# Kernel optimization log

Hardware: AMD Instinct MI355X
Metric: run time of the kernel (lower is better)

Reference implementation:

```python
import jax, jax.numpy as jnp
import numpy as np

B, N, E = 2, 50000, 400000
FIN, HID, OUT = 128, 128, 128
EPS = 1e-5  # BatchNorm1d default eps


def setup_inputs() -> dict:
    key = jax.random.key(0)
    ks = jax.random.split(key, 12)
    x = jax.random.normal(ks[0], (B, N, FIN), dtype=jnp.float32)
    row = jax.random.randint(ks[1], (E,), 0, N, dtype=jnp.int32)          # scatter dst
    col = jnp.concatenate([jnp.arange(N, dtype=jnp.int32),                # ensure deg>=1
                           jax.random.randint(ks[2], (E - N,), 0, N, dtype=jnp.int32)])
    edge_index = jnp.stack([row, col])                                    # [2, E]
    deg = jnp.zeros((N,), jnp.float32).at[col].add(1.0)                   # degree(col, N)
    dis = deg ** -0.5
    norm = (dis[row] * dis[col])[None, :, None]                           # [1, E, 1]
    W1 = jax.random.normal(ks[3], (HID, FIN), jnp.float32) / np.sqrt(FIN)
    b1 = jax.random.normal(ks[4], (HID,), jnp.float32) * 0.01
    g1 = jnp.ones((N,), jnp.float32)
    be1 = jnp.zeros((N,), jnp.float32)
    W2 = jax.random.normal(ks[5], (OUT, HID), jnp.float32) / np.sqrt(HID)
    b2 = jax.random.normal(ks[6], (OUT,), jnp.float32) * 0.01
    g2 = jnp.ones((N,), jnp.float32)
    be2 = jnp.zeros((N,), jnp.float32)
    return {"x": x, "edge_index": edge_index, "norm": norm,
            "W1": W1, "b1": b1, "g1": g1, "be1": be1,
            "W2": W2, "b2": b2, "g2": g2, "be2": be2}


def _gcn_layer(x, edge_index, norm, W, b, g, be):
    # Linear (dropout p=0 -> identity)
    h = jnp.einsum('bnf,of->bno', x, W) + b                 # [B, N, C]
    # BatchNorm1d(num_features=N): per-node stats over (batch, channel)
    mu = jnp.mean(h, axis=(0, 2), keepdims=True)            # [1, N, 1]
    var = jnp.var(h, axis=(0, 2), keepdims=True)            # biased, as torch
    y = g[None, :, None] * (h - mu) * jax.lax.rsqrt(var + EPS) + be[None, :, None]
    a = jax.nn.gelu(y, approximate=False)                   # torch GELU = exact erf
    # message passing: gather src nodes, scale by norm, scatter-add to dst
    msgs = a[:, edge_index[1], :] * norm                    # [B, E, C]
    return jnp.zeros_like(a).at[:, edge_index[0], :].add(msgs)


def reference(x, edge_index, norm, W1, b1, g1, be1, W2, b2, g2, be2):
    x = _gcn_layer(x, edge_index, norm, W1, b1, g1, be1)
    x = _gcn_layer(x, edge_index, norm, W2, b2, g2, be2)
    return x
```

## Files before the change

kernel.cpp:

```cpp
#include <hip/hip_runtime.h>
#include <math.h>

#define CC 128

typedef unsigned short u16;
typedef short bf16x8 __attribute__((ext_vector_type(8)));
typedef float f32x4 __attribute__((ext_vector_type(4)));

typedef __attribute__((address_space(3))) void lds_t;
typedef const __attribute__((address_space(1))) void gbl_t;

__device__ __forceinline__ u16 f2bf(float f) {
    union { float f; unsigned u; } v; v.f = f;
    unsigned u = v.u;
    return (u16)((u + 0x7FFFu + ((u >> 16) & 1u)) >> 16);
}
__device__ __forceinline__ float bf2f(unsigned hi16) {
    union { unsigned u; float f; } v; v.u = hi16 << 16; return v.f;
}
__device__ __forceinline__ unsigned cvt_pk(float lo, float hi) {
    unsigned r;
    asm("v_cvt_pk_bf16_f32 %0, %1, %2" : "=v"(r) : "v"(lo), "v"(hi));
    return r;
}

__device__ __forceinline__ float gelu_f(float y) {
    float xa = fabsf(y) * 0.70710678118654752f;
    float t  = __builtin_amdgcn_rcpf(fmaf(0.3275911f, xa, 1.0f));
    float p  = fmaf(1.061405429f, t, -1.453152027f);
    p = fmaf(p, t, 1.421413741f);
    p = fmaf(p, t, -0.284496736f);
    p = fmaf(p, t, 0.254829592f);
    p *= t;
    float e  = __expf(-xa * xa);
    float er = fmaf(-p, e, 1.0f);
    float s  = copysignf(er, y);
    return 0.5f * y * (1.0f + s);
}


__global__ __launch_bounds__(256) void k_zero_i32(int* __restrict__ p, int n) {
    int i = blockIdx.x * 256 + threadIdx.x;
    if (i < n) p[i] = 0;
}

__global__ __launch_bounds__(256) void k_hist(const int* __restrict__ row, int* __restrict__ cnt, int E) {
    int e = blockIdx.x * 256 + threadIdx.x;
    if (e < E) atomicAdd(&cnt[row[e]], 1);
}

__device__ __forceinline__ int wave_incl_scan(int v) {
    #pragma unroll
    for (int d = 1; d < 64; d <<= 1) {
        int t = __shfl_up(v, d);
        if ((threadIdx.x & 63) >= d) v += t;
    }
    return v;
}

__global__ __launch_bounds__(256) void k_scan_a(const int* __restrict__ cnt, int* __restrict__ bsum, int N) {
    int base = blockIdx.x * 1024 + threadIdx.x * 4;
    int s = 0;
    #pragma unroll
    for (int u = 0; u < 4; ++u) { int i = base + u; if (i < N) s += cnt[i]; }
    #pragma unroll
    for (int d = 32; d > 0; d >>= 1) s += __shfl_down(s, d);
    __shared__ int wsum[4];
    if ((threadIdx.x & 63) == 0) wsum[threadIdx.x >> 6] = s;
    __syncthreads();
    if (threadIdx.x == 0) bsum[blockIdx.x] = wsum[0] + wsum[1] + wsum[2] + wsum[3];
}

__global__ __launch_bounds__(64) void k_scan_b(const int* __restrict__ bsum, int* __restrict__ boff,
                                               int* __restrict__ off, int N, int nb) {
    int carry = 0;
    for (int base = 0; base < nb; base += 64) {
        int t = base + (int)threadIdx.x;
        int v = (t < nb) ? bsum[t] : 0;
        int incl = wave_incl_scan(v);
        if (t < nb) boff[t] = carry + incl - v;
        carry += __shfl(incl, 63);
    }
    if (threadIdx.x == 0) off[N] = carry;
}

__global__ __launch_bounds__(256) void k_scan_c(int* __restrict__ cnt, const int* __restrict__ boff,
                                                int* __restrict__ off, int N) {
    int t = threadIdx.x;
    int base = blockIdx.x * 1024 + t * 4;
    int v[4]; int s = 0;
    #pragma unroll
    for (int u = 0; u < 4; ++u) { int i = base + u; v[u] = (i < N) ? cnt[i] : 0; s += v[u]; }
    int incl = wave_incl_scan(s);
    __shared__ int wsum[4];
    int w = t >> 6, lane = t & 63;
    if (lane == 63) wsum[w] = incl;
    __syncthreads();
    int run = incl - s + boff[blockIdx.x];
    for (int ww = 0; ww < w; ++ww) run += wsum[ww];
    #pragma unroll
    for (int u = 0; u < 4; ++u) {
        int i = base + u;
        if (i < N) { off[i] = run; cnt[i] = 0; }
        run += v[u];
    }
}

__global__ __launch_bounds__(256) void k_fill(const int* __restrict__ row, const int* __restrict__ col,
                                              const float* __restrict__ nrm, const int* __restrict__ off,
                                              int* __restrict__ cur, int2* __restrict__ eg, int E) {
    int e = blockIdx.x * 256 + threadIdx.x;
    if (e < E) {
        int r = row[e];
        int p = off[r] + atomicAdd(&cur[r], 1);
        eg[p] = make_int2(col[e], __float_as_int(nrm[e]));
    }
}

__global__ __launch_bounds__(256) void k_wrepack(const float* __restrict__ W1, u16* __restrict__ Wp1,
                                                 const float* __restrict__ W2, u16* __restrict__ Wp2) {
    int i = blockIdx.x * 256 + threadIdx.x;
    if (i < 2 * CC * CC) {
        int is2 = (i >= CC * CC);
        int ii = is2 ? i - CC * CC : i;
        int j = ii & 7, l = (ii >> 3) & 63, s = (ii >> 9) & 3, t = ii >> 11;
        int r = 16 * t + (l & 15);
        int p = s * 32 + ((l >> 4) & 3) * 8 + j;
        if (is2) {
            int k = (p & 7) * 16 + (p >> 3);
            Wp2[ii] = f2bf(W2[r * CC + k]);
        } else {
            Wp1[ii] = f2bf(W1[r * CC + p]);
        }
    }
}

__global__ __launch_bounds__(256) void k_fused_l1(
    const float* __restrict__ X, const u16* __restrict__ Wp1, const u16* __restrict__ Wp2,
    const float* __restrict__ bias, const float* __restrict__ gamma, const float* __restrict__ beta,
    u16* __restrict__ Z, int N)
{
    __shared__ __align__(16) u16 WS[CC * CC];
    __shared__ __align__(16) unsigned TT[4][16][68];

    const int tid = threadIdx.x;
    const int w = tid >> 6;
    const int l = tid & 63;
    const int g = l >> 4;
    const int c = l & 15;
    const int n8 = blockIdx.x * 32 + w * 8;
    const bool valid = n8 < N;
    const int nbase = valid ? n8 : 0;

    #pragma unroll
    for (int it = 0; it < 8; ++it) {
        const u16* gsrc = Wp1 + it * 2048 + w * 512 + l * 8;
        u16* ldst = &WS[it * 2048 + w * 512];
        __builtin_amdgcn_global_load_lds((gbl_t*)gsrc, (lds_t*)ldst, 16, 0, 0);
    }

    const int ab = c >> 3;
    const int an = nbase + (c & 7);
    const float* xbase = X + ((size_t)ab * N + an) * CC + g * 8;
    bf16x8 af[4];
    #pragma unroll
    for (int s = 0; s < 4; ++s) {
        float4 lo = *(const float4*)(xbase + s * 32);
        float4 hi = *(const float4*)(xbase + s * 32 + 4);
        unsigned aw[4];
        aw[0] = cvt_pk(lo.x, lo.y); aw[1] = cvt_pk(lo.z, lo.w);
        aw[2] = cvt_pk(hi.x, hi.y); aw[3] = cvt_pk(hi.z, hi.w);
        af[s] = *(bf16x8*)aw;
    }

    float bb[8];
    #pragma unroll
    for (int t = 0; t < 8; ++t) bb[t] = bias[t * 16 + c];
    float gam[4], bet[4];
    #pragma unroll
    for (int r = 0; r < 4; ++r) {
        int p = (4 * g + r) & 7;
        gam[r] = gamma[nbase + p];
        bet[r] = beta[nbase + p];
    }

    __syncthreads();

    f32x4 acc[8];
    #pragma unroll
    for (int t = 0; t < 8; ++t) acc[t] = (f32x4){0.f, 0.f, 0.f, 0.f};
    #pragma unroll
    for (int s = 0; s < 4; ++s) {
        bf16x8 bf[8];
        #pragma unroll
        for (int t = 0; t < 8; ++t)
            bf[t] = *(const bf16x8*)&WS[((t * 4 + s) * 64 + l) * 8];
        #pragma unroll
        for (int t = 0; t < 8; ++t)
            acc[t] = __builtin_amdgcn_mfma_f32_16x16x32_bf16(af[s], bf[t], acc[t], 0, 0, 0);
    }

    __syncthreads();

    #pragma unroll
    for (int it = 0; it < 8; ++it) {
        const u16* gsrc = Wp2 + it * 2048 + w * 512 + l * 8;
        u16* ldst = &WS[it * 2048 + w * 512];
        __builtin_amdgcn_global_load_lds((gbl_t*)gsrc, (lds_t*)ldst, 16, 0, 0);
    }

    float rs[4] = {0.f, 0.f, 0.f, 0.f}, rq[4] = {0.f, 0.f, 0.f, 0.f};
    #pragma unroll
    for (int t = 0; t < 8; ++t)
        #pragma unroll
        for (int r = 0; r < 4; ++r) {
            float h = acc[t][r] + bb[t];
            acc[t][r] = h;
            rs[r] += h;
            rq[r] += h * h;
        }
    #pragma unroll
    for (int d = 1; d < 16; d <<= 1) {
        #pragma unroll
        for (int r = 0; r < 4; ++r) {
            rs[r] += __shfl_xor(rs[r], d);
            rq[r] += __shfl_xor(rq[r], d);
        }
    }
    #pragma unroll
    for (int r = 0; r < 4; ++r) {
        rs[r] += __shfl_xor(rs[r], 32);
        rq[r] += __shfl_xor(rq[r], 32);
    }

    #pragma unroll
    for (int r = 0; r < 4; ++r) {
        float mean = rs[r] * (1.f / 256.f);
        float var  = rq[r] * (1.f / 256.f) - mean * mean;
        float sc = gam[r] * rsqrtf(fmaxf(var, 0.f) + 1e-5f);
        float sh = bet[r] - mean * sc;
        #pragma unroll
        for (int t = 0; t < 8; ++t)
            acc[t][r] = gelu_f(acc[t][r] * sc + sh);
    }

    #pragma unroll
    for (int r = 0; r < 4; ++r) {
        unsigned tw[4];
        #pragma unroll
        for (int tt = 0; tt < 4; ++tt)
            tw[tt] = cvt_pk(acc[2 * tt][r], acc[2 * tt + 1][r]);
        *(uint4*)&TT[w][4 * g + r][c * 4] = *(uint4*)tw;
    }
    bf16x8 af2[4];
    #pragma unroll
    for (int s = 0; s < 4; ++s)
        af2[s] = *(const bf16x8*)&TT[w][c][s * 16 + g * 4];

    __syncthreads();

    f32x4 acc2[8];
    #pragma unroll
    for (int t = 0; t < 8; ++t) acc2[t] = (f32x4){0.f, 0.f, 0.f, 0.f};
    #pragma unroll
    for (int s = 0; s < 4; ++s) {
        bf16x8 bf[8];
        #pragma unroll
        for (int t = 0; t < 8; ++t)
            bf[t] = *(const bf16x8*)&WS[((t * 4 + s) * 64 + l) * 8];
        #pragma unroll
        for (int t = 0; t < 8; ++t)
            acc2[t] = __builtin_amdgcn_mfma_f32_16x16x32_bf16(af2[s], bf[t], acc2[t], 0, 0, 0);
    }

    if (valid) {
        #pragma unroll
        for (int r = 0; r < 4; ++r) {
            int rr = 4 * g + r;
            int db = rr >> 3, dn = n8 + (rr & 7);
            unsigned zw[4];
            #pragma unroll
            for (int tt = 0; tt < 4; ++tt)
                zw[tt] = cvt_pk(acc2[2 * tt][r], acc2[2 * tt + 1][r]);
            *(uint4*)(Z + ((size_t)db * N + dn) * CC + c * 8) = *(uint4*)zw;
        }
    }
}

__global__ __launch_bounds__(256) void k_agg_bn(
    const u16* __restrict__ Zin, const int* __restrict__ off, const int2* __restrict__ eg,
    const float* __restrict__ b2, const float* __restrict__ g2, const float* __restrict__ be2,
    u16* __restrict__ A2, int N)
{
    int n = blockIdx.x * 4 + (threadIdx.x >> 6);
    if (n >= N) return;
    int l = threadIdx.x & 63;
    int p = l >> 5;
    int b = (l >> 4) & 1;
    int c = l & 15;
    const u16* Ab = Zin + (size_t)b * N * CC + c * 8;
    int s = off[n], e = off[n + 1];
    float a[8] = {0.f, 0.f, 0.f, 0.f, 0.f, 0.f, 0.f, 0.f};
    for (int j = s; j < e; j += 8) {
        int i0 = j + p, i1 = j + 2 + p, i2 = j + 4 + p, i3 = j + 6 + p;
        int2 e0 = (i0 < e) ? eg[i0] : make_int2(0, 0);
        int2 e1 = (i1 < e) ? eg[i1] : make_int2(0, 0);
        int2 e2 = (i2 < e) ? eg[i2] : make_int2(0, 0);
        int2 e3 = (i3 < e) ? eg[i3] : make_int2(0, 0);
        bf16x8 v0 = *(const bf16x8*)(Ab + (size_t)e0.x * CC);
        bf16x8 v1 = *(const bf16x8*)(Ab + (size_t)e1.x * CC);
        bf16x8 v2 = *(const bf16x8*)(Ab + (size_t)e2.x * CC);
        bf16x8 v3 = *(const bf16x8*)(Ab + (size_t)e3.x * CC);
        float w0 = __int_as_float(e0.y), w1 = __int_as_float(e1.y);
        float w2 = __int_as_float(e2.y), w3 = __int_as_float(e3.y);
        #pragma unroll
        for (int q = 0; q < 8; ++q) {
            a[q] = fmaf(w0, bf2f((u16)v0[q]), a[q]);
            a[q] = fmaf(w1, bf2f((u16)v1[q]), a[q]);
            a[q] = fmaf(w2, bf2f((u16)v2[q]), a[q]);
            a[q] = fmaf(w3, bf2f((u16)v3[q]), a[q]);
        }
    }
    #pragma unroll
    for (int q = 0; q < 8; ++q) a[q] += __shfl_xor(a[q], 32);

    float ss = 0.f, qq = 0.f;
    #pragma unroll
    for (int t = 0; t < 8; ++t) {
        float h = a[t] + b2[t * 16 + c];
        a[t] = h;
        ss += h;
        qq += h * h;
    }
    #pragma unroll
    for (int d = 1; d < 32; d <<= 1) {
        ss += __shfl_xor(ss, d);
        qq += __shfl_xor(qq, d);
    }
    float mean = ss * (1.f / 256.f);
    float var  = qq * (1.f / 256.f) - mean * mean;
    float sc = g2[n] * rsqrtf(fmaxf(var, 0.f) + 1e-5f);
    float sh = be2[n] - mean * sc;

    if (l < 32) {
        unsigned ow[4];
        #pragma unroll
        for (int tt = 0; tt < 4; ++tt) {
            float y0 = gelu_f(a[2 * tt] * sc + sh);
            float y1 = gelu_f(a[2 * tt + 1] * sc + sh);
            ow[tt] = cvt_pk(y0, y1);
        }
        *(uint4*)(A2 + ((size_t)b * N + n) * CC + c * 8) = *(uint4*)ow;
    }
}

__global__ __launch_bounds__(256) void k_agg_out(
    const u16* __restrict__ A2, const int* __restrict__ off, const int2* __restrict__ eg,
    float* __restrict__ Out, int N)
{
    int n = blockIdx.x * 4 + (threadIdx.x >> 6);
    if (n >= N) return;
    int l = threadIdx.x & 63;
    int p = l >> 5;
    int b = (l >> 4) & 1;
    int c = l & 15;
    const u16* Ab = A2 + (size_t)b * N * CC + c * 8;
    int s = off[n], e = off[n + 1];
    float a[8] = {0.f, 0.f, 0.f, 0.f, 0.f, 0.f, 0.f, 0.f};
    for (int j = s; j < e; j += 8) {
        int i0 = j + p, i1 = j + 2 + p, i2 = j + 4 + p, i3 = j + 6 + p;
        int2 e0 = (i0 < e) ? eg[i0] : make_int2(0, 0);
        int2 e1 = (i1 < e) ? eg[i1] : make_int2(0, 0);
        int2 e2 = (i2 < e) ? eg[i2] : make_int2(0, 0);
        int2 e3 = (i3 < e) ? eg[i3] : make_int2(0, 0);
        bf16x8 v0 = *(const bf16x8*)(Ab + (size_t)e0.x * CC);
        bf16x8 v1 = *(const bf16x8*)(Ab + (size_t)e1.x * CC);
        bf16x8 v2 = *(const bf16x8*)(Ab + (size_t)e2.x * CC);
        bf16x8 v3 = *(const bf16x8*)(Ab + (size_t)e3.x * CC);
        float w0 = __int_as_float(e0.y), w1 = __int_as_float(e1.y);
        float w2 = __int_as_float(e2.y), w3 = __int_as_float(e3.y);
        #pragma unroll
        for (int q = 0; q < 8; ++q) {
            a[q] = fmaf(w0, bf2f((u16)v0[q]), a[q]);
            a[q] = fmaf(w1, bf2f((u16)v1[q]), a[q]);
            a[q] = fmaf(w2, bf2f((u16)v2[q]), a[q]);
            a[q] = fmaf(w3, bf2f((u16)v3[q]), a[q]);
        }
    }
    #pragma unroll
    for (int q = 0; q < 8; ++q) a[q] += __shfl_xor(a[q], 32);
    if (l < 32) {
        float* d = Out + ((size_t)b * N + n) * CC + c;
        #pragma unroll
        for (int t = 0; t < 8; ++t) d[t * 16] = a[t];
    }
}


extern "C" void kernel_launch(void* const* d_in, const int* in_sizes, int n_in,
                              void* d_out, int out_size, void* d_ws, size_t ws_size,
                              hipStream_t stream)
{
    const float* x   = (const float*)d_in[0];
    const int*   ei  = (const int*)d_in[1];
    const float* nrm = (const float*)d_in[2];
    const float* W1  = (const float*)d_in[3];
    const float* b1  = (const float*)d_in[4];
    const float* g1  = (const float*)d_in[5];
    const float* be1 = (const float*)d_in[6];
    const float* W2  = (const float*)d_in[7];
    const float* b2  = (const float*)d_in[8];
    const float* g2  = (const float*)d_in[9];
    const float* be2 = (const float*)d_in[10];

    const int N = in_sizes[5];
    const int E = in_sizes[2];
    const int* row = ei;
    const int* col = ei + E;
    const int nb = (N + 1023) / 1024;

    auto al = [](size_t v) { return (v + 255) & ~(size_t)255; };
    char* p = (char*)d_ws;
    int* off    = (int*)p;   p += al((size_t)(N + 1) * 4);
    int* cur    = (int*)p;   p += al((size_t)N * 4);
    int2* eg    = (int2*)p;  p += al((size_t)E * 8);
    int* bsum   = (int*)p;   p += al((size_t)nb * 4);
    int* boff   = (int*)p;   p += al((size_t)nb * 4);
    u16* Wp1    = (u16*)p;   p += al((size_t)CC * CC * 2);
    u16* Wp2    = (u16*)p;   p += al((size_t)CC * CC * 2);
    u16* Zbuf   = (u16*)p;   p += al((size_t)2 * N * CC * 2);
    u16* A2buf  = (u16*)p;   p += al((size_t)2 * N * CC * 2);

    k_zero_i32<<<(N + 255) / 256, 256, 0, stream>>>(cur, N);
    k_hist<<<(E + 255) / 256, 256, 0, stream>>>(row, cur, E);
    k_scan_a<<<nb, 256, 0, stream>>>(cur, bsum, N);
    k_scan_b<<<1, 64, 0, stream>>>(bsum, boff, off, N, nb);
    k_scan_c<<<nb, 256, 0, stream>>>(cur, boff, off, N);
    k_fill<<<(E + 255) / 256, 256, 0, stream>>>(row, col, nrm, off, cur, eg, E);

    k_wrepack<<<(2 * CC * CC + 255) / 256, 256, 0, stream>>>(W1, Wp1, W2, Wp2);

    const int gb = (N + 31) / 32;
    const int ga = (N + 3) / 4;
    k_fused_l1<<<gb, 256, 0, stream>>>(x, Wp1, Wp2, b1, g1, be1, Zbuf, N);
    k_agg_bn<<<ga, 256, 0, stream>>>(Zbuf, off, eg, b2, g2, be2, A2buf, N);
    k_agg_out<<<ga, 256, 0, stream>>>(A2buf, off, eg, (float*)d_out, N);
}
```

Before: 160.6 us.

## Interleave batches per node in intermediates and vectorize output stores

The Z and A2 intermediates switch from batch-major [B][N][C] to node-major [N][B][C]. Each gathered neighbour row now covers both batches in one contiguous 512-byte span instead of two separate 256-byte rows, which should improve coalescing and cache-line use in both aggregation kernels. k_agg_bn goes through a small per-wave LDS buffer to write A2 in logical channel order, so k_agg_out can store fp32 output as float4 vectors instead of strided scalars. The cost is extra LDS traffic and an intra-wave LDS write-then-read with no explicit barrier.

```diff
diff --git a/kernel.cpp b/kernel.cpp
--- a/kernel.cpp
+++ b/kernel.cpp
@@ -282,7 +282,7 @@
             #pragma unroll
             for (int tt = 0; tt < 4; ++tt)
                 zw[tt] = cvt_pk(acc2[2 * tt][r], acc2[2 * tt + 1][r]);
-            *(uint4*)(Z + ((size_t)db * N + dn) * CC + c * 8) = *(uint4*)zw;
+            *(uint4*)(Z + ((size_t)dn * 2 + db) * CC + c * 8) = *(uint4*)zw;
         }
     }
 }
@@ -292,13 +292,15 @@
     const float* __restrict__ b2, const float* __restrict__ g2, const float* __restrict__ be2,
     u16* __restrict__ A2, int N)
 {
-    int n = blockIdx.x * 4 + (threadIdx.x >> 6);
+    __shared__ u16 TW[4][256];
+    int wv = threadIdx.x >> 6;
+    int n = blockIdx.x * 4 + wv;
     if (n >= N) return;
     int l = threadIdx.x & 63;
     int p = l >> 5;
     int b = (l >> 4) & 1;
     int c = l & 15;
-    const u16* Ab = Zin + (size_t)b * N * CC + c * 8;
+    const u16* Ab = Zin + b * CC + c * 8;
     int s = off[n], e = off[n + 1];
     float a[8] = {0.f, 0.f, 0.f, 0.f, 0.f, 0.f, 0.f, 0.f};
     for (int j = s; j < e; j += 8) {
@@ -307,10 +309,10 @@
         int2 e1 = (i1 < e) ? eg[i1] : make_int2(0, 0);
         int2 e2 = (i2 < e) ? eg[i2] : make_int2(0, 0);
         int2 e3 = (i3 < e) ? eg[i3] : make_int2(0, 0);
-        bf16x8 v0 = *(const bf16x8*)(Ab + (size_t)e0.x * CC);
-        bf16x8 v1 = *(const bf16x8*)(Ab + (size_t)e1.x * CC);
-        bf16x8 v2 = *(const bf16x8*)(Ab + (size_t)e2.x * CC);
-        bf16x8 v3 = *(const bf16x8*)(Ab + (size_t)e3.x * CC);
+        bf16x8 v0 = *(const bf16x8*)(Ab + (size_t)e0.x * 256);
+        bf16x8 v1 = *(const bf16x8*)(Ab + (size_t)e1.x * 256);
+        bf16x8 v2 = *(const bf16x8*)(Ab + (size_t)e2.x * 256);
+        bf16x8 v3 = *(const bf16x8*)(Ab + (size_t)e3.x * 256);
         float w0 = __int_as_float(e0.y), w1 = __int_as_float(e1.y);
         float w2 = __int_as_float(e2.y), w3 = __int_as_float(e3.y);
         #pragma unroll
@@ -343,14 +345,13 @@
     float sh = be2[n] - mean * sc;
 
     if (l < 32) {
-        unsigned ow[4];
-        #pragma unroll
-        for (int tt = 0; tt < 4; ++tt) {
-            float y0 = gelu_f(a[2 * tt] * sc + sh);
-            float y1 = gelu_f(a[2 * tt + 1] * sc + sh);
-            ow[tt] = cvt_pk(y0, y1);
-        }
-        *(uint4*)(A2 + ((size_t)b * N + n) * CC + c * 8) = *(uint4*)ow;
+        #pragma unroll
+        for (int t = 0; t < 8; ++t)
+            TW[wv][b * CC + t * 16 + c] = f2bf(gelu_f(a[t] * sc + sh));
+    }
+    if (l < 32) {
+        bf16x8 v = *(const bf16x8*)&TW[wv][l * 8];
+        *(bf16x8*)(A2 + (size_t)n * 256 + l * 8) = v;
     }
 }
 
@@ -362,9 +363,8 @@
     if (n >= N) return;
     int l = threadIdx.x & 63;
     int p = l >> 5;
-    int b = (l >> 4) & 1;
-    int c = l & 15;
-    const u16* Ab = A2 + (size_t)b * N * CC + c * 8;
+    int sl = l & 31;
+    const u16* Ab = A2 + sl * 8;
     int s = off[n], e = off[n + 1];
     float a[8] = {0.f, 0.f, 0.f, 0.f, 0.f, 0.f, 0.f, 0.f};
     for (int j = s; j < e; j += 8) {
@@ -373,10 +373,10 @@
         int2 e1 = (i1 < e) ? eg[i1] : make_int2(0, 0);
         int2 e2 = (i2 < e) ? eg[i2] : make_int2(0, 0);
         int2 e3 = (i3 < e) ? eg[i3] : make_int2(0, 0);
-        bf16x8 v0 = *(const bf16x8*)(Ab + (size_t)e0.x * CC);
-        bf16x8 v1 = *(const bf16x8*)(Ab + (size_t)e1.x * CC);
-        bf16x8 v2 = *(const bf16x8*)(Ab + (size_t)e2.x * CC);
-        bf16x8 v3 = *(const bf16x8*)(Ab + (size_t)e3.x * CC);
+        bf16x8 v0 = *(const bf16x8*)(Ab + (size_t)e0.x * 256);
+        bf16x8 v1 = *(const bf16x8*)(Ab + (size_t)e1.x * 256);
+        bf16x8 v2 = *(const bf16x8*)(Ab + (size_t)e2.x * 256);
+        bf16x8 v3 = *(const bf16x8*)(Ab + (size_t)e3.x * 256);
         float w0 = __int_as_float(e0.y), w1 = __int_as_float(e1.y);
         float w2 = __int_as_float(e2.y), w3 = __int_as_float(e3.y);
         #pragma unroll
@@ -390,9 +390,11 @@
     #pragma unroll
     for (int q = 0; q < 8; ++q) a[q] += __shfl_xor(a[q], 32);
     if (l < 32) {
-        float* d = Out + ((size_t)b * N + n) * CC + c;
-        #pragma unroll
-        for (int t = 0; t < 8; ++t) d[t * 16] = a[t];
+        int b = sl >> 4;
+        int ch0 = (sl & 15) * 8;
+        float* d = Out + ((size_t)b * N + n) * CC + ch0;
+        *(float4*)&d[0] = make_float4(a[0], a[1], a[2], a[3]);
+        *(float4*)&d[4] = make_float4(a[4], a[5], a[6], a[7]);
     }
 }
 
```

Measured after the change: 161.0 us. About the same (+0.3%).
